# Performance work log

Measured on AMD Instinct MI355X. Metric: run time of the kernel, lower is better.

The kernel has to match this reference:

```python
import jax, jax.numpy as jnp
import numpy as np

N_HEADS = 16
D_MODEL = 1024
D_K = D_MODEL // N_HEADS


def setup_inputs() -> dict:
    key = jax.random.key(0)
    ks = jax.random.split(key, 7)
    B, S = 2, 2048
    init = 0.02
    return {
        "query": jax.random.normal(ks[0], (B, S, D_MODEL), dtype=jnp.float32),
        "key": jax.random.normal(ks[1], (B, S, D_MODEL), dtype=jnp.float32),
        "value": jax.random.normal(ks[2], (B, S, D_MODEL), dtype=jnp.float32),
        "W_q": jax.random.normal(ks[3], (D_MODEL, D_MODEL), dtype=jnp.float32) * init,
        "W_k": jax.random.normal(ks[4], (D_MODEL, D_MODEL), dtype=jnp.float32) * init,
        "W_v": jax.random.normal(ks[5], (D_MODEL, D_MODEL), dtype=jnp.float32) * init,
        "W_o": jax.random.normal(ks[6], (D_MODEL, D_MODEL), dtype=jnp.float32) * init,
    }


def _split_heads(x):
    # (B, S, d_model) -> (B, H, S, d_k)
    B, S, _ = x.shape
    return x.reshape(B, S, N_HEADS, D_K).transpose(0, 2, 1, 3)


def reference(query, key, value, W_q, W_k, W_v, W_o):
    scale = jnp.sqrt(jnp.asarray(D_K, dtype=query.dtype))
    # torch Linear: y = x @ W.T
    Q = _split_heads(query @ W_q.T)   # (B,H,Sq,dk)
    K = _split_heads(key @ W_k.T)     # (B,H,Sk,dk)
    V = _split_heads(value @ W_v.T)   # (B,H,Sk,dk)
    scores = jnp.einsum("bhqd,bhkd->bhqk", Q, K) / scale
    attn = jax.nn.softmax(scores, axis=-1)           # (B,H,Sq,Sk); dropout p=0 -> identity
    attn_weights = attn.mean(axis=1)                 # (B,Sq,Sk) interpretable weights
    head_out = jnp.einsum("bhqk,bhkd->bqhd", attn, V)  # (B,Sq,H,dk)
    # NOTE: the original computes a head-gating (W_h) whose result is overwritten
    # by the concat below -> dead code, omitted.
    B, Sq = head_out.shape[0], head_out.shape[1]
    out = head_out.reshape(B, Sq, D_MODEL) @ W_o.T   # (B,Sq,d_model)
    return (out, attn_weights)
```

## Files before the change

### kernel.cpp

```cpp
#include <hip/hip_runtime.h>
#include <hip/hip_bf16.h>

#define Bq 2
#define Hh 16
#define Ss 2048
#define Dm 1024
#define Dk 64
#define QSC 0.18033688f

typedef _Float16 f16x8 __attribute__((ext_vector_type(8)));
typedef _Float16 f16x4 __attribute__((ext_vector_type(4)));
typedef _Float16 f16x2 __attribute__((ext_vector_type(2)));
typedef float    f32x4 __attribute__((ext_vector_type(4)));


__device__ __forceinline__ void gl_lds16(const void* g, void* lds) {
    __builtin_amdgcn_global_load_lds(
        (const __attribute__((address_space(1))) void*)g,
        (__attribute__((address_space(3))) void*)lds, 16, 0, 0);
}

extern "C" __device__ float __ocml_exp2_f32(float);

__device__ __forceinline__ float exp2_fast(float x) {
#if __has_builtin(__builtin_amdgcn_exp2f)
    return __builtin_amdgcn_exp2f(x);
#else
    return __ocml_exp2_f32(x);
#endif
}

__device__ __forceinline__ float rcp_fast(float x) {
#if __has_builtin(__builtin_amdgcn_rcpf)
    return __builtin_amdgcn_rcpf(x);
#else
    float r; asm("v_rcp_f32 %0, %1" : "=v"(r) : "v"(x)); return r;
#endif
}

__device__ __forceinline__ f16x2 pk_f16(float a, float b) {
    return __builtin_bit_cast(f16x2, __builtin_amdgcn_cvt_pkrtz(a, b));
}

__global__ __launch_bounds__(256) void convert_kernel(
    const float* __restrict__ q, const float* __restrict__ k,
    const float* __restrict__ v, const float* __restrict__ wq,
    const float* __restrict__ wk, const float* __restrict__ wv,
    const float* __restrict__ wo,
    _Float16* __restrict__ qd, _Float16* __restrict__ kd,
    _Float16* __restrict__ vd, _Float16* __restrict__ wd)
{
    int seg = blockIdx.y;
    const float* src; _Float16* dst; int n4;
    switch (seg) {
        case 0: src = q; dst = qd; n4 = 1048576; break;
        case 1: src = k; dst = kd; n4 = 1048576; break;
        case 2: src = v; dst = vd; n4 = 1048576; break;
        default:
            src = (seg == 3) ? wq : (seg == 4) ? wk : (seg == 5) ? wv : wo;
            dst = wd + (size_t)(seg - 3) * 1048576;
            n4 = 262144;
    }
    for (int i = blockIdx.x * 256 + threadIdx.x; i < n4; i += gridDim.x * 256) {
        float4 x = ((const float4*)src)[i];
        f16x4 h = {(_Float16)x.x, (_Float16)x.y, (_Float16)x.z, (_Float16)x.w};
        ((f16x4*)dst)[i] = h;
    }
}

__global__ __launch_bounds__(256) void gemm_qkv(
    const _Float16* __restrict__ qf, const _Float16* __restrict__ kf,
    const _Float16* __restrict__ vf, const _Float16* __restrict__ Wh,
    _Float16* __restrict__ Qd, _Float16* __restrict__ Kd,
    _Float16* __restrict__ Vd)
{
    __shared__ alignas(16) char smem[32768];
    _Float16* As = (_Float16*)smem;
    _Float16* Ws = (_Float16*)(smem + 8192);
    int z = blockIdx.z;
    const _Float16* A = (z == 0) ? qf : (z == 1) ? kf : vf;
    const _Float16* W = Wh + (size_t)z * (Dm * Dm);
    int t = threadIdx.x, lane = t & 63, w = t >> 6;
    int quad = lane >> 4, l15 = lane & 15;
    int wm = w & 1, wn = w >> 1;
    int orig = blockIdx.y * 8 + blockIdx.x;
    int wgid = (orig & 7) * 32 + (orig >> 3);
    int n0 = (wgid & 7) * 128, m0 = (wgid >> 3) * 128;

    f32x4 acc[4][4] = {};
    for (int k0 = 0; k0 < Dm; k0 += 32) {
        __syncthreads();
        for (int j = 0; j < 2; ++j) {
            int ca = w * 128 + j * 64 + lane;
            int row = ca >> 2, c8 = (ca & 3) * 8;
            gl_lds16(&A[(size_t)(m0 + row) * Dm + k0 + c8],
                     &As[(size_t)(w * 128 + j * 64) * 8]);
            gl_lds16(&W[(size_t)(n0 + row) * Dm + k0 + c8],
                     &Ws[(size_t)(w * 128 + j * 64) * 8]);
        }
        __syncthreads();
        f16x8 af[4], bf[4];
        for (int mi = 0; mi < 4; ++mi)
            af[mi] = *(const f16x8*)&As[(wm * 64 + mi * 16 + l15) * 32 + quad * 8];
        for (int ni = 0; ni < 4; ++ni)
            bf[ni] = *(const f16x8*)&Ws[(wn * 64 + ni * 16 + l15) * 32 + quad * 8];
        for (int mi = 0; mi < 4; ++mi)
            for (int ni = 0; ni < 4; ++ni)
                acc[mi][ni] = __builtin_amdgcn_mfma_f32_16x16x32_f16(
                    af[mi], bf[ni], acc[mi][ni], 0, 0, 0);
    }

    if (z == 2) {
        __syncthreads();
        for (int mi = 0; mi < 4; ++mi)
            for (int ni = 0; ni < 4; ++ni) {
                int n_l = wn * 64 + ni * 16 + l15;
                int m_b = wm * 64 + mi * 16 + quad * 4;
                f16x4 hv = {(_Float16)acc[mi][ni][0], (_Float16)acc[mi][ni][1],
                            (_Float16)acc[mi][ni][2], (_Float16)acc[mi][ni][3]};
                *(f16x4*)(smem + n_l * 256 + ((m_b * 2) ^ ((n_l & 7) << 4))) = hv;
            }
        __syncthreads();
        int b = m0 >> 11, sb = m0 & (Ss - 1);
        for (int p = 0; p < 8; ++p) {
            int cid = p * 256 + t;
            int rown = cid >> 4, c16 = cid & 15;
            f16x8 v = *(const f16x8*)(smem + rown * 256 +
                                      ((c16 * 16) ^ ((rown & 7) << 4)));
            int n = n0 + rown;
            int h = n >> 6, d = n & 63;
            *(f16x8*)&Vd[(((size_t)(b * Hh + h) * Dk + d) << 11) + sb + c16 * 8] = v;
        }
    } else {
        _Float16* Y = (z == 0) ? Qd : Kd;
        float osc = (z == 0) ? QSC : 1.0f;
        for (int mi = 0; mi < 4; ++mi)
            for (int ni = 0; ni < 4; ++ni)
                for (int r = 0; r < 4; ++r) {
                    int m = m0 + wm * 64 + mi * 16 + quad * 4 + r;
                    int n = n0 + wn * 64 + ni * 16 + l15;
                    int b = m >> 11, s = m & (Ss - 1);
                    int h = n >> 6,  d = n & 63;
                    Y[(((size_t)(b * Hh + h) * Ss + s) << 6) + d] =
                        (_Float16)(acc[mi][ni][r] * osc);
                }
    }
}

__global__ __launch_bounds__(256) void flash_kernel(
    const _Float16* __restrict__ Qh, const _Float16* __restrict__ Kh,
    const _Float16* __restrict__ Vt, _Float16* __restrict__ Op,
    float* __restrict__ lp)
{
    __shared__ alignas(16) char Ks[8192];
    __shared__ alignas(16) char Vs[8192];
    __shared__ alignas(16) char Ps[4][4096];
    int t = threadIdx.x;
    int lane = t & 63, w = t >> 6;
    int quad = lane >> 4, l15 = lane & 15;
    int bh = blockIdx.x;
    int q0 = blockIdx.y * 128 + w * 32;
    int ks = blockIdx.z;
    int kt0 = ks * 16, kt1 = kt0 + 16;

    const _Float16* Qp = Qh + (size_t)bh * Ss * Dk;
    const _Float16* Kp = Kh + (size_t)bh * Ss * Dk;
    const _Float16* Vp = Vt + (size_t)bh * Dk * Ss;

    f16x8 qf[2][2];
#pragma unroll
    for (int qh = 0; qh < 2; ++qh)
#pragma unroll
        for (int kf = 0; kf < 2; ++kf)
            qf[qh][kf] = *(const f16x8*)
                &Qp[(size_t)(q0 + qh * 16 + l15) * Dk + kf * 32 + quad * 8];

    const _Float16 one = (_Float16)1.0f;
    const f16x8 ones = {one, one, one, one, one, one, one, one};

    int srow0 = t >> 3;
    int colh  = (t & 7) * 8;
    int sw0 = srow0 * 128 + ((colh * 2) ^ ((srow0 & 7) << 4));
    int sw1 = sw0 + 32 * 128;
    int swz = (l15 & 7) << 4;

    f16x8 kr0 = *(const f16x8*)&Kp[(size_t)(kt0 * 64 + srow0) * Dk + colh];
    f16x8 kr1 = *(const f16x8*)&Kp[(size_t)(kt0 * 64 + srow0 + 32) * Dk + colh];
    f16x8 vr0 = *(const f16x8*)&Vp[(size_t)srow0 * Ss + kt0 * 64 + colh];
    f16x8 vr1 = *(const f16x8*)&Vp[(size_t)(srow0 + 32) * Ss + kt0 * 64 + colh];

    f32x4 o_acc[2][4] = {};
    f32x4 l_acc[2] = {};
    char* Pw = Ps[w];

    for (int kt = kt0; kt < kt1; ++kt) {
        __syncthreads();
        *(f16x8*)(Ks + sw0) = kr0;
        *(f16x8*)(Ks + sw1) = kr1;
        *(f16x8*)(Vs + sw0) = vr0;
        *(f16x8*)(Vs + sw1) = vr1;
        if (kt + 1 < kt1) {
            kr0 = *(const f16x8*)&Kp[(size_t)((kt + 1) * 64 + srow0) * Dk + colh];
            kr1 = *(const f16x8*)&Kp[(size_t)((kt + 1) * 64 + srow0 + 32) * Dk + colh];
            vr0 = *(const f16x8*)&Vp[(size_t)srow0 * Ss + (kt + 1) * 64 + colh];
            vr1 = *(const f16x8*)&Vp[(size_t)(srow0 + 32) * Ss + (kt + 1) * 64 + colh];
        }
        __syncthreads();

#pragma unroll
        for (int nt = 0; nt < 4; ++nt) {
            const char* rb = Ks + ((nt * 16 + l15) << 7);
            f16x8 kf0 = *(const f16x8*)(rb + ((quad * 16) ^ swz));
            f16x8 kf1 = *(const f16x8*)(rb + ((64 + quad * 16) ^ swz));
#pragma unroll
            for (int qh = 0; qh < 2; ++qh) {
                f32x4 z = {};
                z = __builtin_amdgcn_mfma_f32_16x16x32_f16(kf0, qf[qh][0], z, 0, 0, 0);
                z = __builtin_amdgcn_mfma_f32_16x16x32_f16(kf1, qf[qh][1], z, 0, 0, 0);
                f16x2 h0 = pk_f16(exp2_fast(z[0]), exp2_fast(z[1]));
                f16x2 h1 = pk_f16(exp2_fast(z[2]), exp2_fast(z[3]));
                f16x4 hv = {h0[0], h0[1], h1[0], h1[1]};
                int prow = qh * 16 + l15;
                *(f16x4*)(Pw + prow * 128 +
                          (((nt * 32 + quad * 8)) ^ ((prow & 7) << 4))) = hv;
            }
        }

        f16x8 vf[4][2];
#pragma unroll
        for (int dt = 0; dt < 4; ++dt) {
            const char* rb = Vs + ((dt * 16 + l15) << 7);
            vf[dt][0] = *(const f16x8*)(rb + ((quad * 16) ^ swz));
            vf[dt][1] = *(const f16x8*)(rb + ((64 + quad * 16) ^ swz));
        }
#pragma unroll
        for (int qh = 0; qh < 2; ++qh) {
            const char* pr = Pw + ((qh * 16 + l15) << 7);
            f16x8 pf0 = *(const f16x8*)(pr + ((quad * 16) ^ swz));
            f16x8 pf1 = *(const f16x8*)(pr + ((64 + quad * 16) ^ swz));
            l_acc[qh] = __builtin_amdgcn_mfma_f32_16x16x32_f16(
                pf0, ones, l_acc[qh], 0, 0, 0);
            l_acc[qh] = __builtin_amdgcn_mfma_f32_16x16x32_f16(
                pf1, ones, l_acc[qh], 0, 0, 0);
#pragma unroll
            for (int dt = 0; dt < 4; ++dt) {
                o_acc[qh][dt] = __builtin_amdgcn_mfma_f32_16x16x32_f16(
                    pf0, vf[dt][0], o_acc[qh][dt], 0, 0, 0);
                o_acc[qh][dt] = __builtin_amdgcn_mfma_f32_16x16x32_f16(
                    pf1, vf[dt][1], o_acc[qh][dt], 0, 0, 0);
            }
        }
    }

    _Float16* Od = Op + (size_t)ks * (Bq * Hh * Ss * Dk) + (size_t)bh * Ss * Dk;
#pragma unroll
    for (int qh = 0; qh < 2; ++qh) {
#pragma unroll
        for (int dt = 0; dt < 4; ++dt)
#pragma unroll
            for (int r = 0; r < 4; ++r) {
                int q = q0 + qh * 16 + quad * 4 + r;
                Od[(size_t)q * Dk + dt * 16 + l15] = (_Float16)o_acc[qh][dt][r];
            }
        if (l15 == 0)
#pragma unroll
            for (int r = 0; r < 4; ++r)
                lp[(size_t)ks * 65536 + (size_t)bh * Ss + q0 + qh * 16 +
                   quad * 4 + r] = l_acc[qh][r];
    }
}

__global__ __launch_bounds__(256) void reduce_kernel(
    const _Float16* __restrict__ Op, const float* __restrict__ lp,
    _Float16* __restrict__ HO, float* __restrict__ lw)
{
    int i = blockIdx.x * 256 + threadIdx.x;
    int d4  = i & 15;
    int row = i >> 4;
    f16x4 a = ((const f16x4*)Op)[i];
    f16x4 b = ((const f16x4*)Op)[i + 1048576];
    float l = lp[row] + lp[65536 + row];
    float inv = rcp_fast(l);
    int bh = row >> 11, q = row & (Ss - 1);
    int b_ = bh >> 4,  h = bh & 15;
    f16x4 o;
    for (int j = 0; j < 4; ++j)
        o[j] = (_Float16)(((float)a[j] + (float)b[j]) * inv);
    *(f16x4*)&HO[((size_t)(b_ * Ss + q)) * Dm + h * Dk + d4 * 4] = o;
    if (d4 == 0) lw[row] = l;
}

__global__ __launch_bounds__(256) void tail_kernel(
    const _Float16* __restrict__ HO, const _Float16* __restrict__ Woh,
    float* __restrict__ out, const _Float16* __restrict__ Qh,
    const _Float16* __restrict__ Kh, const float* __restrict__ lw,
    float* __restrict__ out_attn)
{
    __shared__ alignas(16) char smem[12288];
    int id = blockIdx.x;
    int t = threadIdx.x, lane = t & 63, w = t >> 6;
    int quad = lane >> 4, l15 = lane & 15;

    if (id % 3 == 0) {
        int go = id / 3;
        _Float16* As = (_Float16*)smem;
        _Float16* Ws = (_Float16*)(smem + 8192);
        int n0 = (go & 15) * 64, m0 = (go >> 4) * 128;

        f32x4 acc[2][4] = {};
        for (int k0 = 0; k0 < Dm; k0 += 32) {
            __syncthreads();
            for (int j = 0; j < 2; ++j) {
                int ca = w * 128 + j * 64 + lane;
                int row = ca >> 2, c8 = (ca & 3) * 8;
                gl_lds16(&HO[(size_t)(m0 + row) * Dm + k0 + c8],
                         &As[(size_t)(w * 128 + j * 64) * 8]);
            }
            {
                int cw = w * 64 + lane;
                int row = cw >> 2, c8 = (cw & 3) * 8;
                gl_lds16(&Woh[(size_t)(n0 + row) * Dm + k0 + c8],
                         &Ws[(size_t)(w * 64) * 8]);
            }
            __syncthreads();
            f16x8 af[2], bf[4];
            for (int mi = 0; mi < 2; ++mi)
                af[mi] = *(const f16x8*)&As[(w * 32 + mi * 16 + l15) * 32 + quad * 8];
            for (int ni = 0; ni < 4; ++ni)
                bf[ni] = *(const f16x8*)&Ws[(ni * 16 + l15) * 32 + quad * 8];
            for (int mi = 0; mi < 2; ++mi)
                for (int ni = 0; ni < 4; ++ni)
                    acc[mi][ni] = __builtin_amdgcn_mfma_f32_16x16x32_f16(
                        af[mi], bf[ni], acc[mi][ni], 0, 0, 0);
        }
        for (int mi = 0; mi < 2; ++mi)
            for (int ni = 0; ni < 4; ++ni)
                for (int r = 0; r < 4; ++r) {
                    int m = m0 + w * 32 + mi * 16 + quad * 4 + r;
                    int n = n0 + ni * 16 + l15;
                    out[(size_t)m * Dm + n] = acc[mi][ni][r];
                }
    } else {
        int am = id - id / 3 - 1;
        char* Ks = smem;
        int k0 = (am & 31) * 64;
        int q0 = ((am >> 5) & 15) * 128;
        int b  = am >> 9;
        int qrow = q0 + w * 32;

        int srow0 = t >> 3;
        int colh  = (t & 7) * 8;
        int sw0 = srow0 * 128 + ((colh * 2) ^ ((srow0 & 7) << 4));
        int sw1 = sw0 + 32 * 128;
        int swz = (l15 & 7) << 4;

        f16x8 kr0, kr1, qn[2][2];
        float4 ln[2];
        {
            size_t base = (size_t)(b * Hh) * Ss;
            kr0 = *(const f16x8*)&Kh[(base + k0 + srow0) * Dk + colh];
            kr1 = *(const f16x8*)&Kh[(base + k0 + srow0 + 32) * Dk + colh];
#pragma unroll
            for (int qh = 0; qh < 2; ++qh) {
                qn[qh][0] = *(const f16x8*)&Qh[(base + qrow + qh * 16 + l15) * Dk + quad * 8];
                qn[qh][1] = *(const f16x8*)&Qh[(base + qrow + qh * 16 + l15) * Dk + 32 + quad * 8];
                ln[qh] = *(const float4*)&lw[base + qrow + qh * 16 + quad * 4];
            }
        }

        f32x4 acc[2][4] = {};
        for (int h = 0; h < Hh; ++h) {
            __syncthreads();
            *(f16x8*)(Ks + sw0) = kr0;
            *(f16x8*)(Ks + sw1) = kr1;
            f16x8 qf[2][2];
            float4 lv[2];
#pragma unroll
            for (int qh = 0; qh < 2; ++qh) {
                qf[qh][0] = qn[qh][0]; qf[qh][1] = qn[qh][1]; lv[qh] = ln[qh];
            }
            if (h < Hh - 1) {
                size_t base = (size_t)(b * Hh + h + 1) * Ss;
                kr0 = *(const f16x8*)&Kh[(base + k0 + srow0) * Dk + colh];
                kr1 = *(const f16x8*)&Kh[(base + k0 + srow0 + 32) * Dk + colh];
#pragma unroll
                for (int qh = 0; qh < 2; ++qh) {
                    qn[qh][0] = *(const f16x8*)&Qh[(base + qrow + qh * 16 + l15) * Dk + quad * 8];
                    qn[qh][1] = *(const f16x8*)&Qh[(base + qrow + qh * 16 + l15) * Dk + 32 + quad * 8];
                    ln[qh] = *(const float4*)&lw[base + qrow + qh * 16 + quad * 4];
                }
            }
            __syncthreads();

            float ir[2][4];
#pragma unroll
            for (int qh = 0; qh < 2; ++qh) {
                ir[qh][0] = rcp_fast(lv[qh].x); ir[qh][1] = rcp_fast(lv[qh].y);
                ir[qh][2] = rcp_fast(lv[qh].z); ir[qh][3] = rcp_fast(lv[qh].w);
            }
#pragma unroll
            for (int nt = 0; nt < 4; ++nt) {
                const char* rb = Ks + ((nt * 16 + l15) << 7);
                f16x8 b0 = *(const f16x8*)(rb + ((quad * 16) ^ swz));
                f16x8 b1 = *(const f16x8*)(rb + ((64 + quad * 16) ^ swz));
#pragma unroll
                for (int qh = 0; qh < 2; ++qh) {
                    f32x4 z = {};
                    z = __builtin_amdgcn_mfma_f32_16x16x32_f16(qf[qh][0], b0, z, 0, 0, 0);
                    z = __builtin_amdgcn_mfma_f32_16x16x32_f16(qf[qh][1], b1, z, 0, 0, 0);
#pragma unroll
                    for (int r = 0; r < 4; ++r)
                        acc[qh][nt][r] += exp2_fast(z[r]) * ir[qh][r];
                }
            }
        }

#pragma unroll
        for (int qh = 0; qh < 2; ++qh)
#pragma unroll
            for (int nt = 0; nt < 4; ++nt)
#pragma unroll
                for (int r = 0; r < 4; ++r) {
                    int q = qrow + qh * 16 + quad * 4 + r;
                    out_attn[((size_t)(b * Ss + q)) * Ss + k0 + nt * 16 + l15] =
                        acc[qh][nt][r] * (1.0f / Hh);
                }
    }
}

extern "C" void kernel_launch(void* const* d_in, const int* in_sizes, int n_in,
                              void* d_out, int out_size, void* d_ws, size_t ws_size,
                              hipStream_t stream) {
    const float* query = (const float*)d_in[0];
    const float* key   = (const float*)d_in[1];
    const float* value = (const float*)d_in[2];
    const float* Wq    = (const float*)d_in[3];
    const float* Wk    = (const float*)d_in[4];
    const float* Wv    = (const float*)d_in[5];
    const float* Wo    = (const float*)d_in[6];

    float* out      = (float*)d_out;
    float* attn_out = out + (size_t)4194304;

    _Float16* qf  = (_Float16*)(attn_out + 2097152);
    _Float16* kf  = qf + 4194304;
    _Float16* vf  = kf + 4194304;
    _Float16* Op  = qf;
    float*    lp  = (float*)(Op + 2 * 4194304);

    _Float16* Qh = (_Float16*)d_ws;
    _Float16* Kh = Qh + (size_t)4194304;
    _Float16* Vt = Kh + (size_t)4194304;
    _Float16* Wh = Vt + (size_t)4194304;
    float*    lw = (float*)(Wh + (size_t)4194304);
    _Float16* HO = Vt;

    convert_kernel<<<dim3(256, 7), 256, 0, stream>>>(
        query, key, value, Wq, Wk, Wv, Wo, qf, kf, vf, Wh);

    gemm_qkv<<<dim3(8, 32, 3), 256, 0, stream>>>(qf, kf, vf, Wh, Qh, Kh, Vt);

    flash_kernel<<<dim3(Bq * Hh, Ss / 128, 2), 256, 0, stream>>>(Qh, Kh, Vt, Op, lp);

    reduce_kernel<<<4096, 256, 0, stream>>>(Op, lp, HO, lw);

    tail_kernel<<<1536, 256, 0, stream>>>(
        HO, Wh + (size_t)3 * 1048576, out, Qh, Kh, lw, attn_out);
}
```

Baseline: 256.9 us.

## Widen QKV GEMM K-tile to 64 with swizzled LDS; double-buffer K in tail

The QKV projection GEMM now loads a 64-wide K slice per iteration instead of 32. Its LDS tiles use an XOR swizzle to avoid bank conflicts, and it runs two MFMA sub-steps per sync pair, halving barrier count. In the tail attention-weights path, the K tile is double-buffered by head parity so one of the two barriers per head can be dropped. This raises LDS usage in the tail kernel, which may lower occupancy.

Result: slower. 263.6 us (+2.6%).

```diff
diff --git a/kernel.cpp b/kernel.cpp
--- a/kernel.cpp
+++ b/kernel.cpp
@@ -75,8 +75,8 @@
     _Float16* __restrict__ Vd)
 {
     __shared__ alignas(16) char smem[32768];
-    _Float16* As = (_Float16*)smem;
-    _Float16* Ws = (_Float16*)(smem + 8192);
+    char* As = smem;
+    char* Ws = smem + 16384;
     int z = blockIdx.z;
     const _Float16* A = (z == 0) ? qf : (z == 1) ? kf : vf;
     const _Float16* W = Wh + (size_t)z * (Dm * Dm);
@@ -88,26 +88,41 @@
     int n0 = (wgid & 7) * 128, m0 = (wgid >> 3) * 128;
 
     f32x4 acc[4][4] = {};
-    for (int k0 = 0; k0 < Dm; k0 += 32) {
-        __syncthreads();
-        for (int j = 0; j < 2; ++j) {
-            int ca = w * 128 + j * 64 + lane;
-            int row = ca >> 2, c8 = (ca & 3) * 8;
-            gl_lds16(&A[(size_t)(m0 + row) * Dm + k0 + c8],
-                     &As[(size_t)(w * 128 + j * 64) * 8]);
-            gl_lds16(&W[(size_t)(n0 + row) * Dm + k0 + c8],
-                     &Ws[(size_t)(w * 128 + j * 64) * 8]);
-        }
-        __syncthreads();
-        f16x8 af[4], bf[4];
-        for (int mi = 0; mi < 4; ++mi)
-            af[mi] = *(const f16x8*)&As[(wm * 64 + mi * 16 + l15) * 32 + quad * 8];
-        for (int ni = 0; ni < 4; ++ni)
-            bf[ni] = *(const f16x8*)&Ws[(wn * 64 + ni * 16 + l15) * 32 + quad * 8];
-        for (int mi = 0; mi < 4; ++mi)
-            for (int ni = 0; ni < 4; ++ni)
-                acc[mi][ni] = __builtin_amdgcn_mfma_f32_16x16x32_f16(
-                    af[mi], bf[ni], acc[mi][ni], 0, 0, 0);
+    for (int k0 = 0; k0 < Dm; k0 += 64) {
+        __syncthreads();
+#pragma unroll
+        for (int j = 0; j < 4; ++j) {
+            int ca = j * 256 + t;
+            int row = ca >> 3, cb = (ca & 7) * 16;
+            int sc = cb ^ ((row & 7) << 4);
+            gl_lds16((const char*)&A[(size_t)(m0 + row) * Dm + k0] + sc,
+                     As + ca * 16);
+            gl_lds16((const char*)&W[(size_t)(n0 + row) * Dm + k0] + sc,
+                     Ws + ca * 16);
+        }
+        __syncthreads();
+#pragma unroll
+        for (int kk = 0; kk < 2; ++kk) {
+            f16x8 af[4], bf[4];
+#pragma unroll
+            for (int mi = 0; mi < 4; ++mi) {
+                int row = wm * 64 + mi * 16 + l15;
+                af[mi] = *(const f16x8*)(As + row * 128 +
+                          ((kk * 64 + quad * 16) ^ ((row & 7) << 4)));
+            }
+#pragma unroll
+            for (int ni = 0; ni < 4; ++ni) {
+                int row = wn * 64 + ni * 16 + l15;
+                bf[ni] = *(const f16x8*)(Ws + row * 128 +
+                          ((kk * 64 + quad * 16) ^ ((row & 7) << 4)));
+            }
+#pragma unroll
+            for (int mi = 0; mi < 4; ++mi)
+#pragma unroll
+                for (int ni = 0; ni < 4; ++ni)
+                    acc[mi][ni] = __builtin_amdgcn_mfma_f32_16x16x32_f16(
+                        af[mi], bf[ni], acc[mi][ni], 0, 0, 0);
+        }
     }
 
     if (z == 2) {
@@ -296,7 +311,7 @@
     const _Float16* __restrict__ Kh, const float* __restrict__ lw,
     float* __restrict__ out_attn)
 {
-    __shared__ alignas(16) char smem[12288];
+    __shared__ alignas(16) char smem[16384];
     int id = blockIdx.x;
     int t = threadIdx.x, lane = t & 63, w = t >> 6;
     int quad = lane >> 4, l15 = lane & 15;
@@ -370,9 +385,9 @@
 
         f32x4 acc[2][4] = {};
         for (int h = 0; h < Hh; ++h) {
-            __syncthreads();
-            *(f16x8*)(Ks + sw0) = kr0;
-            *(f16x8*)(Ks + sw1) = kr1;
+            char* Kb = Ks + (h & 1) * 8192;
+            *(f16x8*)(Kb + sw0) = kr0;
+            *(f16x8*)(Kb + sw1) = kr1;
             f16x8 qf[2][2];
             float4 lv[2];
 #pragma unroll
@@ -400,7 +415,7 @@
             }
 #pragma unroll
             for (int nt = 0; nt < 4; ++nt) {
-                const char* rb = Ks + ((nt * 16 + l15) << 7);
+                const char* rb = Kb + ((nt * 16 + l15) << 7);
                 f16x8 b0 = *(const f16x8*)(rb + ((quad * 16) ^ swz));
                 f16x8 b1 = *(const f16x8*)(rb + ((64 + quad * 16) ^ swz));
 #pragma unroll
```
